# Kernel tuning notes

Hardware: AMD Instinct MI355X
Metric: run time of the kernel (lower is better)

Reference implementation:

```python
import jax, jax.numpy as jnp
import numpy as np

B, C, N, F = 256, 4, 64, 256   # batch, in_channels, neighbors, in_features
OC, OF = 8, 256                # out_channels, out_features


def setup_inputs() -> dict:
    key = jax.random.key(0)
    k1, k2, k3, k4, k5 = jax.random.split(key, 5)
    x = jax.random.normal(k1, (B, C, F), dtype=jnp.float32)
    neighbor = jax.random.normal(k2, (B, N, C, F), dtype=jnp.float32)
    # torch.nn.Linear weights are (out_features, in_features)
    W_att1 = jax.random.normal(k3, (C, F), dtype=jnp.float32) / np.sqrt(F).astype(np.float32)
    W_att2 = jax.random.normal(k4, (C, F), dtype=jnp.float32) / np.sqrt(F).astype(np.float32)
    # Conv1d weight: (out_c*out_f, 2C, F); kernel_size==F makes it a dense contraction
    W_conv = jax.random.normal(k5, (OC * OF, 2 * C, F), dtype=jnp.float32) / np.sqrt(2 * C * F).astype(np.float32)
    return {"x": x, "neighbor": neighbor, "W_att1": W_att1, "W_att2": W_att2, "W_conv": W_conv}


def reference(x, neighbor, W_att1, W_att2, W_conv):
    # --- attention weights: einsum 'ci,nkl->n' = sum(att1(x_i)) * sum_{k,l} att2(y_i)[n]
    s1 = jnp.sum(x @ W_att1.T, axis=(1, 2))              # (B,)
    s2 = jnp.sum(neighbor @ W_att2.T, axis=(2, 3))       # (B, N)
    w = jax.nn.softmax(s1[:, None] * s2, axis=1)         # softmax over neighbors (dim 0 per-sample)

    # --- feature adjacency: einsum 'ca,ncb,n->cab' vectorized over batch
    fadj = jnp.einsum('bcx,bncy,bn->bcxy', x, neighbor, w)   # (B, C, F, F)
    fadj = fadj + jnp.swapaxes(fadj, -1, -2)
    # sgnroot
    fadj = jnp.sign(fadj) * jnp.sqrt(jnp.clip(jnp.abs(fadj), 1e-8, None))
    # row normalize over dim -2, NaN -> 0
    adj = fadj / (jnp.abs(fadj).sum(axis=-2, keepdims=True) + 1e-7)
    adj = jnp.where(jnp.isnan(adj), jnp.float32(0.0), adj)

    # --- transform: cat([adj @ x, x], channel) then full-width conv1d (dense contraction)
    h = jnp.einsum('bcxy,bcy->bcx', adj, x)              # (B, C, F)
    z = jnp.concatenate([h, x], axis=1)                  # (B, 2C, F)
    out = jnp.einsum('bcf,ocf->bo', z, W_conv).reshape(B, OC, OF)
    return out, adj
```

## Files before the change

### kernel.cpp

```cpp
#include <hip/hip_runtime.h>
#include <hip/hip_bf16.h>
#include <math.h>


typedef __bf16 bf16x8 __attribute__((ext_vector_type(8)));
typedef __bf16 bf16x4 __attribute__((ext_vector_type(4)));
typedef float f32x4 __attribute__((ext_vector_type(4)));

#define NB 256
#define NC 4
#define NN 64
#define NF 256
#define NO 2048

__global__ __launch_bounds__(256) void k_pre(
    const float* __restrict__ x, const float* __restrict__ nb,
    const float* __restrict__ W1, const float* __restrict__ W2,
    const float* __restrict__ Wc,
    __hip_bfloat16* __restrict__ Wcb, __hip_bfloat16* __restrict__ zbf,
    float* __restrict__ s1, float* __restrict__ s2)
{
  __shared__ float w2s[256], w1s[256];
  int t = threadIdx.x;
  int w = t >> 6, l = t & 63;

  w2s[t] = W2[t] + W2[256 + t] + W2[512 + t] + W2[768 + t];
  w1s[t] = W1[t] + W1[256 + t] + W1[512 + t] + W1[768 + t];
  __syncthreads();

  int gw = blockIdx.x * 4 + w;
  float4 wv2 = *(const float4*)&w2s[l * 4];
  float4 wv1 = *(const float4*)&w1s[l * 4];
  for (int task = gw; task < 16640; task += 8192) {
    bool isS2 = task < 16384;
    const float4* src = isS2 ? ((const float4*)nb + (size_t)task * 256)
                             : ((const float4*)x + (size_t)(task - 16384) * 256);
    float4 wv = isS2 ? wv2 : wv1;
    float val = 0.f;
    #pragma unroll
    for (int k = 0; k < 4; ++k) {
      float4 v = src[l + 64 * k];
      val += v.x * wv.x + v.y * wv.y + v.z * wv.z + v.w * wv.w;
    }
    for (int off = 32; off > 0; off >>= 1) val += __shfl_down(val, off);
    if (l == 0) {
      if (isS2) s2[task] = val;
      else s1[task - 16384] = val;
    }
  }

  for (int task = blockIdx.x; task < 4352; task += 2048) {
    if (task < 4096) {
      int idx = task * 256 + t;
      float4 v = ((const float4*)Wc)[idx];
      bf16x4 o = { (__bf16)v.x, (__bf16)v.y, (__bf16)v.z, (__bf16)v.w };
      ((bf16x4*)Wcb)[idx] = o;
    } else {
      int i = (task - 4096) * 256 + t;
      int e = i * 4;
      int b = e >> 10, r = e & 1023;
      float4 v = ((const float4*)x)[i];
      bf16x4 o = { (__bf16)v.x, (__bf16)v.y, (__bf16)v.z, (__bf16)v.w };
      *(bf16x4*)(zbf + (size_t)b * 2048 + 1024 + r) = o;
    }
  }
}

__global__ __launch_bounds__(256) void k_adj(
    const float* __restrict__ x, const float* __restrict__ nb,
    const float* __restrict__ s1, const float* __restrict__ s2,
    float* __restrict__ adj, __hip_bfloat16* __restrict__ zbf)
{
  __shared__ float xs[256], ns[256], invs[256], wsh[64];
  __shared__ float part[4][256];
  int t = threadIdx.x;
  int w = t >> 6, l = t & 63;
  int blk = blockIdx.x;
  int b = blk >> 2, c = blk & 3;

  if (t < 64) {
    float v = s1[b] * s2[b * 64 + t];
    float m = v;
    for (int off = 32; off > 0; off >>= 1) m = fmaxf(m, __shfl_xor(m, off));
    float e = expf(v - m);
    float s = e;
    for (int off = 32; off > 0; off >>= 1) s += __shfl_xor(s, off);
    wsh[t] = e / s;
  }
  xs[t] = x[(size_t)blk * 256 + t];
  __syncthreads();

  const float4* nb4 = (const float4*)(nb + (size_t)b * 65536 + c * 256);
  float4 a4 = {0.f, 0.f, 0.f, 0.f};
  #pragma unroll
  for (int k = 0; k < 16; ++k) {
    int n = w + 4 * k;
    float4 v = nb4[(size_t)n * 256 + l];
    float wn = wsh[n];
    a4.x = fmaf(wn, v.x, a4.x);
    a4.y = fmaf(wn, v.y, a4.y);
    a4.z = fmaf(wn, v.z, a4.z);
    a4.w = fmaf(wn, v.w, a4.w);
  }
  *(float4*)&part[w][l * 4] = a4;
  __syncthreads();
  ns[t] = part[0][t] + part[1][t] + part[2][t] + part[3][t];
  __syncthreads();

  int j0 = l * 4;
  float4 xv = *(const float4*)&xs[j0];
  float4 nv = *(const float4*)&ns[j0];
  int i0 = w * 64;

  float4 cs = {0.f, 0.f, 0.f, 0.f};
  #pragma unroll 4
  for (int ii = 0; ii < 64; ++ii) {
    int i = i0 + ii;
    float xi = xs[i], ni = ns[i];
    cs.x += __builtin_amdgcn_sqrtf(fmaxf(fabsf(fmaf(xi, nv.x, xv.x * ni)), 1e-8f));
    cs.y += __builtin_amdgcn_sqrtf(fmaxf(fabsf(fmaf(xi, nv.y, xv.y * ni)), 1e-8f));
    cs.z += __builtin_amdgcn_sqrtf(fmaxf(fabsf(fmaf(xi, nv.z, xv.z * ni)), 1e-8f));
    cs.w += __builtin_amdgcn_sqrtf(fmaxf(fabsf(fmaf(xi, nv.w, xv.w * ni)), 1e-8f));
  }
  *(float4*)&part[w][j0] = cs;
  __syncthreads();
  invs[t] = 1.f / (part[0][t] + part[1][t] + part[2][t] + part[3][t] + 1e-7f);
  __syncthreads();

  float4 iv = *(const float4*)&invs[j0];
  float4 ha = {0.f, 0.f, 0.f, 0.f};
  float* ab = adj + (size_t)blk * 65536;
  #pragma unroll 4
  for (int ii = 0; ii < 64; ++ii) {
    int i = i0 + ii;
    float xi = xs[i], ni = ns[i];
    float pix = invs[i] * xi;
    float v0 = fmaf(xi, nv.x, xv.x * ni);
    float v1 = fmaf(xi, nv.y, xv.y * ni);
    float v2 = fmaf(xi, nv.z, xv.z * ni);
    float v3 = fmaf(xi, nv.w, xv.w * ni);
    float g0 = copysignf(__builtin_amdgcn_sqrtf(fmaxf(fabsf(v0), 1e-8f)), v0);
    float g1 = copysignf(__builtin_amdgcn_sqrtf(fmaxf(fabsf(v1), 1e-8f)), v1);
    float g2 = copysignf(__builtin_amdgcn_sqrtf(fmaxf(fabsf(v2), 1e-8f)), v2);
    float g3 = copysignf(__builtin_amdgcn_sqrtf(fmaxf(fabsf(v3), 1e-8f)), v3);
    f32x4 o = { g0 * iv.x, g1 * iv.y, g2 * iv.z, g3 * iv.w };
    __builtin_nontemporal_store(o, (f32x4*)&ab[(size_t)i * 256 + j0]);
    ha.x = fmaf(g0, pix, ha.x);
    ha.y = fmaf(g1, pix, ha.y);
    ha.z = fmaf(g2, pix, ha.z);
    ha.w = fmaf(g3, pix, ha.w);
  }
  __syncthreads();
  *(float4*)&part[w][j0] = ha;
  __syncthreads();
  float hsum = part[0][t] + part[1][t] + part[2][t] + part[3][t];
  zbf[(size_t)b * 2048 + c * 256 + t] = __float2bfloat16(hsum);
}

__global__ __launch_bounds__(256) void k_gemm(
    const __hip_bfloat16* __restrict__ zb, const __hip_bfloat16* __restrict__ Wcb,
    float* __restrict__ out)
{
  __shared__ __hip_bfloat16 Al[64][136];
  __shared__ __hip_bfloat16 Bl[64][136];
  int t = threadIdx.x;
  int wave = t >> 6, lane = t & 63;
  int g = lane >> 4, r = lane & 15;
  int mh = wave >> 1, nh = wave & 1;
  int bm = blockIdx.x & 3, bn = blockIdx.x >> 2;

  f32x4 acc00 = {0.f,0.f,0.f,0.f}, acc01 = {0.f,0.f,0.f,0.f};
  f32x4 acc10 = {0.f,0.f,0.f,0.f}, acc11 = {0.f,0.f,0.f,0.f};

  const float4* zb4 = (const float4*)zb;
  const float4* wc4 = (const float4*)Wcb;

  for (int kb = 0; kb < 16; ++kb) {
    #pragma unroll
    for (int q = 0; q < 4; ++q) {
      int idx = q * 256 + t;
      int row = idx >> 4, c16 = idx & 15;
      float4 va = zb4[(size_t)(bm * 64 + row) * 256 + kb * 16 + c16];
      *(float4*)&Al[row][c16 * 8] = va;
      float4 vb = wc4[(size_t)(bn * 64 + row) * 256 + kb * 16 + c16];
      *(float4*)&Bl[row][c16 * 8] = vb;
    }
    __syncthreads();
    #pragma unroll
    for (int kk = 0; kk < 4; ++kk) {
      bf16x8 a0 = *(const bf16x8*)&Al[mh * 32 + r][kk * 32 + g * 8];
      bf16x8 a1 = *(const bf16x8*)&Al[mh * 32 + 16 + r][kk * 32 + g * 8];
      bf16x8 b0 = *(const bf16x8*)&Bl[nh * 32 + r][kk * 32 + g * 8];
      bf16x8 b1 = *(const bf16x8*)&Bl[nh * 32 + 16 + r][kk * 32 + g * 8];
      acc00 = __builtin_amdgcn_mfma_f32_16x16x32_bf16(a0, b0, acc00, 0, 0, 0);
      acc01 = __builtin_amdgcn_mfma_f32_16x16x32_bf16(a0, b1, acc01, 0, 0, 0);
      acc10 = __builtin_amdgcn_mfma_f32_16x16x32_bf16(a1, b0, acc10, 0, 0, 0);
      acc11 = __builtin_amdgcn_mfma_f32_16x16x32_bf16(a1, b1, acc11, 0, 0, 0);
    }
    __syncthreads();
  }

  int row0 = bm * 64 + mh * 32 + g * 4;
  int col0 = bn * 64 + nh * 32 + r;
  #pragma unroll
  for (int q = 0; q < 4; ++q) {
    __builtin_nontemporal_store(acc00[q], &out[(size_t)(row0 + q) * 2048 + col0]);
    __builtin_nontemporal_store(acc01[q], &out[(size_t)(row0 + q) * 2048 + col0 + 16]);
    __builtin_nontemporal_store(acc10[q], &out[(size_t)(row0 + 16 + q) * 2048 + col0]);
    __builtin_nontemporal_store(acc11[q], &out[(size_t)(row0 + 16 + q) * 2048 + col0 + 16]);
  }
}

__global__ __launch_bounds__(256) void k_scores_fb(
    const float* __restrict__ x, const float* __restrict__ nb,
    const float* __restrict__ W1, const float* __restrict__ W2,
    float* __restrict__ s1, float* __restrict__ s2)
{
  __shared__ float red[4];
  int t = threadIdx.x;
  int gid = blockIdx.x;
  float val;
  if (gid < NB * NN) {
    float w = W2[t] + W2[256 + t] + W2[512 + t] + W2[768 + t];
    const float* p = nb + (size_t)gid * 1024;
    val = w * (p[t] + p[256 + t] + p[512 + t] + p[768 + t]);
  } else {
    int b = gid - NB * NN;
    float w = W1[t] + W1[256 + t] + W1[512 + t] + W1[768 + t];
    const float* p = x + (size_t)b * 1024;
    val = w * (p[t] + p[256 + t] + p[512 + t] + p[768 + t]);
  }
  for (int off = 32; off > 0; off >>= 1) val += __shfl_down(val, off);
  if ((t & 63) == 0) red[t >> 6] = val;
  __syncthreads();
  if (t == 0) {
    float s = red[0] + red[1] + red[2] + red[3];
    if (gid < NB * NN) s2[gid] = s;
    else s1[gid - NB * NN] = s;
  }
}

__global__ __launch_bounds__(256) void k_adj_fb(
    const float* __restrict__ x, const float* __restrict__ nb,
    const float* __restrict__ s1, const float* __restrict__ s2,
    float* __restrict__ adj, float* __restrict__ hf)
{
  __shared__ float xs[256], ns[256], invs[256], wsh[64];
  __shared__ float part[4][256];
  int t = threadIdx.x;
  int w = t >> 6, l = t & 63;
  int blk = blockIdx.x;
  int b = blk >> 2, c = blk & 3;

  if (t < 64) {
    float v = s1[b] * s2[b * 64 + t];
    float m = v;
    for (int off = 32; off > 0; off >>= 1) m = fmaxf(m, __shfl_xor(m, off));
    float e = expf(v - m);
    float s = e;
    for (int off = 32; off > 0; off >>= 1) s += __shfl_xor(s, off);
    wsh[t] = e / s;
  }
  __syncthreads();
  float acc = 0.f;
  const float* pb = nb + (size_t)b * 65536 + c * 256 + t;
  #pragma unroll 8
  for (int n = 0; n < 64; ++n) acc = fmaf(wsh[n], pb[(size_t)n * 1024], acc);
  ns[t] = acc;
  xs[t] = x[(size_t)blk * 256 + t];
  __syncthreads();

  int j0 = l * 4;
  float4 xv = *(const float4*)&xs[j0];
  float4 nv = *(const float4*)&ns[j0];
  int i0 = w * 64;
  float4 cs = {0.f, 0.f, 0.f, 0.f};
  for (int ii = 0; ii < 64; ++ii) {
    int i = i0 + ii;
    float xi = xs[i], ni = ns[i];
    cs.x += __builtin_amdgcn_sqrtf(fmaxf(fabsf(fmaf(xi, nv.x, xv.x * ni)), 1e-8f));
    cs.y += __builtin_amdgcn_sqrtf(fmaxf(fabsf(fmaf(xi, nv.y, xv.y * ni)), 1e-8f));
    cs.z += __builtin_amdgcn_sqrtf(fmaxf(fabsf(fmaf(xi, nv.z, xv.z * ni)), 1e-8f));
    cs.w += __builtin_amdgcn_sqrtf(fmaxf(fabsf(fmaf(xi, nv.w, xv.w * ni)), 1e-8f));
  }
  *(float4*)&part[w][j0] = cs;
  __syncthreads();
  invs[t] = 1.f / (part[0][t] + part[1][t] + part[2][t] + part[3][t] + 1e-7f);
  __syncthreads();

  float4 iv = *(const float4*)&invs[j0];
  float4 ha = {0.f, 0.f, 0.f, 0.f};
  float* ab = adj + (size_t)blk * 65536;
  for (int ii = 0; ii < 64; ++ii) {
    int i = i0 + ii;
    float xi = xs[i], ni = ns[i];
    float pix = invs[i] * xi;
    float v0 = fmaf(xi, nv.x, xv.x * ni);
    float v1 = fmaf(xi, nv.y, xv.y * ni);
    float v2 = fmaf(xi, nv.z, xv.z * ni);
    float v3 = fmaf(xi, nv.w, xv.w * ni);
    float g0 = copysignf(__builtin_amdgcn_sqrtf(fmaxf(fabsf(v0), 1e-8f)), v0);
    float g1 = copysignf(__builtin_amdgcn_sqrtf(fmaxf(fabsf(v1), 1e-8f)), v1);
    float g2 = copysignf(__builtin_amdgcn_sqrtf(fmaxf(fabsf(v2), 1e-8f)), v2);
    float g3 = copysignf(__builtin_amdgcn_sqrtf(fmaxf(fabsf(v3), 1e-8f)), v3);
    f32x4 o = { g0 * iv.x, g1 * iv.y, g2 * iv.z, g3 * iv.w };
    *(f32x4*)&ab[(size_t)i * 256 + j0] = o;
    ha.x = fmaf(g0, pix, ha.x);
    ha.y = fmaf(g1, pix, ha.y);
    ha.z = fmaf(g2, pix, ha.z);
    ha.w = fmaf(g3, pix, ha.w);
  }
  __syncthreads();
  *(float4*)&part[w][j0] = ha;
  __syncthreads();
  hf[(size_t)blk * 256 + t] = part[0][t] + part[1][t] + part[2][t] + part[3][t];
}

__device__ inline bf16x8 cvt8_p(const float* p) {
  const float4* q = reinterpret_cast<const float4*>(p);
  float4 a = q[0], bq = q[1];
  bf16x8 r;
  r[0] = (__bf16)a.x;  r[1] = (__bf16)a.y;  r[2] = (__bf16)a.z;  r[3] = (__bf16)a.w;
  r[4] = (__bf16)bq.x; r[5] = (__bf16)bq.y; r[6] = (__bf16)bq.z; r[7] = (__bf16)bq.w;
  return r;
}

__global__ __launch_bounds__(256) void k_gemm_f32(
    const float* __restrict__ h, const float* __restrict__ x,
    const float* __restrict__ Wc, float* __restrict__ out)
{
  int tid = threadIdx.x;
  int wave = tid >> 6, lane = tid & 63;
  int g = lane >> 4, r = lane & 15;
  int bm = blockIdx.x & 3, bn = blockIdx.x >> 2;
  int m0 = bm * 64 + wave * 16;
  int n0 = bn * 32;
  int arow = m0 + r;
  int koff = g * 8;

  const float* za = h + (size_t)arow * 1024 + koff;
  const float* zb = x + (size_t)arow * 1024 + koff;
  const float* w0 = Wc + (size_t)(n0 + r) * 2048 + koff;
  const float* w1 = Wc + (size_t)(n0 + 16 + r) * 2048 + koff;

  f32x4 acc0 = {0.f, 0.f, 0.f, 0.f}, acc1 = {0.f, 0.f, 0.f, 0.f};
  #pragma unroll 4
  for (int ks = 0; ks < 32; ++ks) {
    acc0 = __builtin_amdgcn_mfma_f32_16x16x32_bf16(cvt8_p(za + ks * 32), cvt8_p(w0 + ks * 32), acc0, 0, 0, 0);
    acc1 = __builtin_amdgcn_mfma_f32_16x16x32_bf16(cvt8_p(za + ks * 32), cvt8_p(w1 + ks * 32), acc1, 0, 0, 0);
  }
  #pragma unroll 4
  for (int ks = 0; ks < 32; ++ks) {
    acc0 = __builtin_amdgcn_mfma_f32_16x16x32_bf16(cvt8_p(zb + ks * 32), cvt8_p(w0 + 1024 + ks * 32), acc0, 0, 0, 0);
    acc1 = __builtin_amdgcn_mfma_f32_16x16x32_bf16(cvt8_p(zb + ks * 32), cvt8_p(w1 + 1024 + ks * 32), acc1, 0, 0, 0);
  }
  #pragma unroll
  for (int q = 0; q < 4; ++q) {
    int row = m0 + g * 4 + q;
    out[(size_t)row * 2048 + n0 + r]      = acc0[q];
    out[(size_t)row * 2048 + n0 + 16 + r] = acc1[q];
  }
}

extern "C" void kernel_launch(void* const* d_in, const int* in_sizes, int n_in,
                              void* d_out, int out_size, void* d_ws, size_t ws_size,
                              hipStream_t stream) {
  const float* x  = (const float*)d_in[0];
  const float* nb = (const float*)d_in[1];
  const float* W1 = (const float*)d_in[2];
  const float* W2 = (const float*)d_in[3];
  const float* Wc = (const float*)d_in[4];
  float* out = (float*)d_out;
  float* adj = out + (size_t)NB * NO;

  char* ws = (char*)d_ws;
  const size_t ZBF_B = 1048576;
  const size_t WCB_B = 8388608;
  const size_t FREG = (256 + 16384) * 4;
  bool fast = ws_size >= ZBF_B + WCB_B + FREG;

  if (fast) {
    __hip_bfloat16* zbf = (__hip_bfloat16*)ws;
    __hip_bfloat16* Wcb = (__hip_bfloat16*)(ws + ZBF_B);
    float* s1  = (float*)(ws + ZBF_B + WCB_B);
    float* s2  = s1 + 256;
    k_pre<<<2048, 256, 0, stream>>>(x, nb, W1, W2, Wc, Wcb, zbf, s1, s2);
    k_adj<<<NB * NC, 256, 0, stream>>>(x, nb, s1, s2, adj, zbf);
    k_gemm<<<128, 256, 0, stream>>>(zbf, Wcb, out);
  } else {
    float* hws = (float*)d_ws;
    float* s1  = hws + 262144;
    float* s2  = s1 + 256;
    k_scores_fb<<<NB * NN + NB, 256, 0, stream>>>(x, nb, W1, W2, s1, s2);
    k_adj_fb<<<NB * NC, 256, 0, stream>>>(x, nb, s1, s2, adj, hws);
    k_gemm_f32<<<256, 256, 0, stream>>>(hws, x, Wc, out);
  }
}
```

Measured before the change: 96.84 us.

## Move weight/x bf16 conversion into k_adj and double-buffer GEMM LDS tiles

Moves the W_conv fp32-to-bf16 conversion and the x-to-bf16 copy out of k_pre and into k_adj. Each of the 1024 k_adj blocks converts its own slice of W_conv, so the conversion traffic shares time with the adjacency computation instead of extending the bandwidth-bound score pass. The GEMM kernel now double-buffers its A/B shared-memory tiles and prefetches the next K-slice into registers during the MFMA loop. In exchange it uses twice the LDS and more registers, and k_adj does extra global traffic per block.

Measured after the change: 95.20 us, median of 2. Within noise of the previous version (-1.7%).

```diff
diff --git a/kernel.cpp b/kernel.cpp
--- a/kernel.cpp
+++ b/kernel.cpp
@@ -16,8 +16,6 @@
 __global__ __launch_bounds__(256) void k_pre(
     const float* __restrict__ x, const float* __restrict__ nb,
     const float* __restrict__ W1, const float* __restrict__ W2,
-    const float* __restrict__ Wc,
-    __hip_bfloat16* __restrict__ Wcb, __hip_bfloat16* __restrict__ zbf,
     float* __restrict__ s1, float* __restrict__ s2)
 {
   __shared__ float w2s[256], w1s[256];
@@ -48,28 +46,14 @@
       else s1[task - 16384] = val;
     }
   }
-
-  for (int task = blockIdx.x; task < 4352; task += 2048) {
-    if (task < 4096) {
-      int idx = task * 256 + t;
-      float4 v = ((const float4*)Wc)[idx];
-      bf16x4 o = { (__bf16)v.x, (__bf16)v.y, (__bf16)v.z, (__bf16)v.w };
-      ((bf16x4*)Wcb)[idx] = o;
-    } else {
-      int i = (task - 4096) * 256 + t;
-      int e = i * 4;
-      int b = e >> 10, r = e & 1023;
-      float4 v = ((const float4*)x)[i];
-      bf16x4 o = { (__bf16)v.x, (__bf16)v.y, (__bf16)v.z, (__bf16)v.w };
-      *(bf16x4*)(zbf + (size_t)b * 2048 + 1024 + r) = o;
-    }
-  }
 }
 
 __global__ __launch_bounds__(256) void k_adj(
     const float* __restrict__ x, const float* __restrict__ nb,
+    const float* __restrict__ Wc,
     const float* __restrict__ s1, const float* __restrict__ s2,
-    float* __restrict__ adj, __hip_bfloat16* __restrict__ zbf)
+    float* __restrict__ adj, __hip_bfloat16* __restrict__ zbf,
+    __hip_bfloat16* __restrict__ Wcb)
 {
   __shared__ float xs[256], ns[256], invs[256], wsh[64];
   __shared__ float part[4][256];
@@ -77,6 +61,18 @@
   int w = t >> 6, l = t & 63;
   int blk = blockIdx.x;
   int b = blk >> 2, c = blk & 3;
+
+  {
+    const float4* Wc4 = (const float4*)Wc;
+    bf16x4* Wcb4 = (bf16x4*)Wcb;
+    #pragma unroll
+    for (int q = 0; q < 4; ++q) {
+      int idx = blk * 1024 + q * 256 + t;
+      float4 v = Wc4[idx];
+      bf16x4 o = { (__bf16)v.x, (__bf16)v.y, (__bf16)v.z, (__bf16)v.w };
+      Wcb4[idx] = o;
+    }
+  }
 
   if (t < 64) {
     float v = s1[b] * s2[b * 64 + t];
@@ -87,7 +83,9 @@
     for (int off = 32; off > 0; off >>= 1) s += __shfl_xor(s, off);
     wsh[t] = e / s;
   }
-  xs[t] = x[(size_t)blk * 256 + t];
+  float xval = x[(size_t)blk * 256 + t];
+  xs[t] = xval;
+  zbf[(size_t)b * 2048 + 1024 + c * 256 + t] = __float2bfloat16(xval);
   __syncthreads();
 
   const float4* nb4 = (const float4*)(nb + (size_t)b * 65536 + c * 256);
@@ -161,8 +159,8 @@
     const __hip_bfloat16* __restrict__ zb, const __hip_bfloat16* __restrict__ Wcb,
     float* __restrict__ out)
 {
-  __shared__ __hip_bfloat16 Al[64][136];
-  __shared__ __hip_bfloat16 Bl[64][136];
+  __shared__ __hip_bfloat16 Al[2][64][136];
+  __shared__ __hip_bfloat16 Bl[2][64][136];
   int t = threadIdx.x;
   int wave = t >> 6, lane = t & 63;
   int g = lane >> 4, r = lane & 15;
@@ -175,29 +173,51 @@
   const float4* zb4 = (const float4*)zb;
   const float4* wc4 = (const float4*)Wcb;
 
+  #pragma unroll
+  for (int q = 0; q < 4; ++q) {
+    int idx = q * 256 + t;
+    int row = idx >> 4, c16 = idx & 15;
+    float4 va = zb4[(size_t)(bm * 64 + row) * 256 + c16];
+    *(float4*)&Al[0][row][c16 * 8] = va;
+    float4 vb = wc4[(size_t)(bn * 64 + row) * 256 + c16];
+    *(float4*)&Bl[0][row][c16 * 8] = vb;
+  }
+  __syncthreads();
+
+  int cur = 0;
   for (int kb = 0; kb < 16; ++kb) {
-    #pragma unroll
-    for (int q = 0; q < 4; ++q) {
-      int idx = q * 256 + t;
-      int row = idx >> 4, c16 = idx & 15;
-      float4 va = zb4[(size_t)(bm * 64 + row) * 256 + kb * 16 + c16];
-      *(float4*)&Al[row][c16 * 8] = va;
-      float4 vb = wc4[(size_t)(bn * 64 + row) * 256 + kb * 16 + c16];
-      *(float4*)&Bl[row][c16 * 8] = vb;
-    }
-    __syncthreads();
+    float4 va[4], vb[4];
+    if (kb < 15) {
+      #pragma unroll
+      for (int q = 0; q < 4; ++q) {
+        int idx = q * 256 + t;
+        int row = idx >> 4, c16 = idx & 15;
+        va[q] = zb4[(size_t)(bm * 64 + row) * 256 + (kb + 1) * 16 + c16];
+        vb[q] = wc4[(size_t)(bn * 64 + row) * 256 + (kb + 1) * 16 + c16];
+      }
+    }
     #pragma unroll
     for (int kk = 0; kk < 4; ++kk) {
-      bf16x8 a0 = *(const bf16x8*)&Al[mh * 32 + r][kk * 32 + g * 8];
-      bf16x8 a1 = *(const bf16x8*)&Al[mh * 32 + 16 + r][kk * 32 + g * 8];
-      bf16x8 b0 = *(const bf16x8*)&Bl[nh * 32 + r][kk * 32 + g * 8];
-      bf16x8 b1 = *(const bf16x8*)&Bl[nh * 32 + 16 + r][kk * 32 + g * 8];
+      bf16x8 a0 = *(const bf16x8*)&Al[cur][mh * 32 + r][kk * 32 + g * 8];
+      bf16x8 a1 = *(const bf16x8*)&Al[cur][mh * 32 + 16 + r][kk * 32 + g * 8];
+      bf16x8 b0 = *(const bf16x8*)&Bl[cur][nh * 32 + r][kk * 32 + g * 8];
+      bf16x8 b1 = *(const bf16x8*)&Bl[cur][nh * 32 + 16 + r][kk * 32 + g * 8];
       acc00 = __builtin_amdgcn_mfma_f32_16x16x32_bf16(a0, b0, acc00, 0, 0, 0);
       acc01 = __builtin_amdgcn_mfma_f32_16x16x32_bf16(a0, b1, acc01, 0, 0, 0);
       acc10 = __builtin_amdgcn_mfma_f32_16x16x32_bf16(a1, b0, acc10, 0, 0, 0);
       acc11 = __builtin_amdgcn_mfma_f32_16x16x32_bf16(a1, b1, acc11, 0, 0, 0);
     }
+    if (kb < 15) {
+      #pragma unroll
+      for (int q = 0; q < 4; ++q) {
+        int idx = q * 256 + t;
+        int row = idx >> 4, c16 = idx & 15;
+        *(float4*)&Al[cur ^ 1][row][c16 * 8] = va[q];
+        *(float4*)&Bl[cur ^ 1][row][c16 * 8] = vb[q];
+      }
+    }
     __syncthreads();
+    cur ^= 1;
   }
 
   int row0 = bm * 64 + mh * 32 + g * 4;
@@ -384,8 +404,8 @@
     __hip_bfloat16* Wcb = (__hip_bfloat16*)(ws + ZBF_B);
     float* s1  = (float*)(ws + ZBF_B + WCB_B);
     float* s2  = s1 + 256;
-    k_pre<<<2048, 256, 0, stream>>>(x, nb, W1, W2, Wc, Wcb, zbf, s1, s2);
-    k_adj<<<NB * NC, 256, 0, stream>>>(x, nb, s1, s2, adj, zbf);
+    k_pre<<<2048, 256, 0, stream>>>(x, nb, W1, W2, s1, s2);
+    k_adj<<<NB * NC, 256, 0, stream>>>(x, nb, Wc, s1, s2, adj, zbf, Wcb);
     k_gemm<<<128, 256, 0, stream>>>(zbf, Wcb, out);
   } else {
     float* hws = (float*)d_ws;
```
